# Optimization experiments

Hardware: AMD Instinct MI355X
Metric: run time of the kernel (lower is better)

The kernel has to match this reference:

```python
import jax, jax.numpy as jnp
import numpy as np

H = 12       # heads
D = 768      # hidden size
DH = D // H  # head dim = 64
SCALE = 1.0 / jnp.sqrt(jnp.float32(DH))
LN_EPS = 1e-3  # keras LayerNormalization default epsilon


def setup_inputs() -> dict:
    key = jax.random.key(0)
    ks = jax.random.split(key, 8)
    B, L = 16, 512
    s = 0.02  # truncated-normal-ish init scale
    return {
        "x": jax.random.normal(ks[0], (B, L, D), jnp.float32),
        "mask": jnp.ones((B, L), jnp.int32),
        "Wq": jax.random.normal(ks[1], (D, D), jnp.float32) * s,
        "bq": jnp.zeros((D,), jnp.float32),
        "Wk": jax.random.normal(ks[2], (D, D), jnp.float32) * s,
        "bk": jnp.zeros((D,), jnp.float32),
        "Wv": jax.random.normal(ks[3], (D, D), jnp.float32) * s,
        "bv": jnp.zeros((D,), jnp.float32),
        "Wo": jax.random.normal(ks[4], (D, D), jnp.float32) * s,
        "bo": jnp.zeros((D,), jnp.float32),
        "gamma": jnp.ones((D,), jnp.float32),
        "beta": jnp.zeros((D,), jnp.float32),
    }


def reference(x, mask, Wq, bq, Wk, bk, Wv, bv, Wo, bo, gamma, beta):
    B, L, _ = x.shape
    # QKV projections, split into heads: [B, L, H, DH]
    q = (x @ Wq + bq).reshape(B, L, H, DH)
    k = (x @ Wk + bk).reshape(B, L, H, DH)
    v = (x @ Wv + bv).reshape(B, L, H, DH)
    # scaled dot-product scores: [B, H, Lq, Lk]
    scores = jnp.einsum('bqhd,bkhd->bhqk', q, k) * SCALE
    # key-side padding mask (mask==0 -> -inf)
    neg = jnp.float32(-1e9)
    scores = jnp.where(mask[:, None, None, :] > 0, scores, neg)
    p = jax.nn.softmax(scores, axis=-1)
    # dropout rate fixed to 0.0 -> identity
    ctx = jnp.einsum('bhqk,bkhd->bqhd', p, v).reshape(B, L, D)
    attn_out = ctx @ Wo + bo
    # residual + LayerNorm (keras default eps=1e-3)
    y = x + attn_out
    mu = jnp.mean(y, axis=-1, keepdims=True)
    var = jnp.mean(jnp.square(y - mu), axis=-1, keepdims=True)
    return gamma * (y - mu) * jax.lax.rsqrt(var + LN_EPS) + beta
```

## Files before the change

kernel.cpp:

```cpp
#include <hip/hip_runtime.h>
#include <math.h>

#define NH 12
#define DMODEL 768
#define DHEAD 64
#define BATCH 16
#define SEQ 512
#define NTOK (BATCH*SEQ)
#define ATTN_SCALE 0.125f
#define LN_EPS 1e-3f
#define PADP 72
#define NKT 12

typedef __attribute__((ext_vector_type(8))) short  bf16x8;
typedef __attribute__((ext_vector_type(4))) float  f32x4;

__device__ __forceinline__ unsigned short f2bf(float f) {
    unsigned int u = __float_as_uint(f);
    unsigned int r = (u + 0x7fffu + ((u >> 16) & 1u)) >> 16;
    return (unsigned short)r;
}

__device__ __forceinline__ void async_copy16(const void* g, void* l) {
    __builtin_amdgcn_global_load_lds((const __attribute__((address_space(1))) void*)g,
                                     (__attribute__((address_space(3))) void*)l,
                                     16, 0, 0);
}

#define SBAR() do { \
    __builtin_amdgcn_sched_barrier(0); \
    __builtin_amdgcn_s_barrier(); \
    __builtin_amdgcn_sched_barrier(0); \
} while (0)

#define VMW0() do { \
    __builtin_amdgcn_sched_barrier(0); \
    asm volatile("s_waitcnt vmcnt(0)" ::: "memory"); \
    __builtin_amdgcn_sched_barrier(0); \
} while (0)

__global__ __launch_bounds__(256) void prep_kernel(
    const float* __restrict__ x,
    const float* __restrict__ Wq, const float* __restrict__ Wk,
    const float* __restrict__ Wv, const float* __restrict__ Wo,
    unsigned short* __restrict__ xb,
    unsigned short* __restrict__ tq, unsigned short* __restrict__ tk,
    unsigned short* __restrict__ tv, unsigned short* __restrict__ to_)
{
    __shared__ float tile[32][33];
    const int bid = blockIdx.x;
    const int tid = threadIdx.x;

    if (bid < 6144) {
        int i = (bid * 256 + tid) * 4;
        const float4 v = *(const float4*)(x + i);
        unsigned long long pack =
              (unsigned long long)f2bf(v.x)
            | ((unsigned long long)f2bf(v.y) << 16)
            | ((unsigned long long)f2bf(v.z) << 32)
            | ((unsigned long long)f2bf(v.w) << 48);
        *(unsigned long long*)(xb + i) = pack;
        return;
    }

    const int t   = bid - 6144;
    const int zz  = t / 576;
    const int rem = t % 576;
    const float* W = (zz == 0) ? Wq : (zz == 1) ? Wk : (zz == 2) ? Wv : Wo;
    unsigned short* T = (zz == 0) ? tq : (zz == 1) ? tk : (zz == 2) ? tv : to_;

    const int bx = (rem / 24) * 32;
    const int by = (rem % 24) * 32;
    const int tx = tid & 31, ty = tid >> 5;

    #pragma unroll
    for (int i = 0; i < 32; i += 8)
        tile[ty + i][tx] = W[(size_t)(bx + ty + i) * DMODEL + by + tx];
    __syncthreads();
    #pragma unroll
    for (int i = 0; i < 32; i += 8)
        T[(size_t)(by + ty + i) * DMODEL + bx + tx] = f2bf(tile[tx][ty + i]);
}

#define QSTAGE(kt, sb) do { \
    const int _k0 = (kt) * 64; \
    _Pragma("unroll") \
    for (int _i = 0; _i < 4; ++_i) \
        async_copy16(aSrc + (size_t)_i * (8 * DMODEL) + _k0, &As[sb][(w * 4 + _i) * 512]); \
    _Pragma("unroll") \
    for (int _i = 0; _i < 4; ++_i) \
        async_copy16(bSrc + (size_t)_i * (64 * DMODEL) + _k0, &Bs[sb][(w + 8 * _i) * 512]); \
    if (w < 4) \
        async_copy16(bSrc + (size_t)4 * (64 * DMODEL) + _k0, &Bs[sb][(w + 32) * 512]); \
} while (0)

#define QTILE(t, c, o, hasNext) do { \
    if (hasNext) QSTAGE((t) + 1, o); \
    bf16x8 aF[4][2]; \
    _Pragma("unroll") \
    for (int _m = 0; _m < 4; ++_m) { \
        const int _row = wm * 64 + _m * 16 + l16; \
        aF[_m][0] = *(const bf16x8*)&As[c][_row * 64 + p0]; \
        aF[_m][1] = *(const bf16x8*)&As[c][_row * 64 + (p0 ^ 32)]; \
    } \
    _Pragma("unroll") \
    for (int _nh = 0; _nh < 3; ++_nh) { \
        bf16x8 bF[3][2]; \
        _Pragma("unroll") \
        for (int _n = 0; _n < 3; ++_n) { \
            const int _row = wn * 144 + (_nh * 3 + _n) * 16 + l16; \
            bF[_n][0] = *(const bf16x8*)&Bs[c][_row * 64 + p0]; \
            bF[_n][1] = *(const bf16x8*)&Bs[c][_row * 64 + (p0 ^ 32)]; \
        } \
        __builtin_amdgcn_s_setprio(1); \
        _Pragma("unroll") \
        for (int _k = 0; _k < 2; ++_k) \
          _Pragma("unroll") \
          for (int _m = 0; _m < 4; ++_m) \
            _Pragma("unroll") \
            for (int _n = 0; _n < 3; ++_n) \
              acc[_m][_nh * 3 + _n] = __builtin_amdgcn_mfma_f32_16x16x32_bf16( \
                  aF[_m][_k], bF[_n][_k], acc[_m][_nh * 3 + _n], 0, 0, 0); \
        __builtin_amdgcn_s_setprio(0); \
    } \
    if (hasNext) VMW0(); \
    SBAR(); \
} while (0)

__global__ __launch_bounds__(512, 2) void gemm_db_qkv(
    const unsigned short* __restrict__ xb, const unsigned short* __restrict__ wt,
    const float* __restrict__ bq, const float* __restrict__ bk, const float* __restrict__ bv,
    unsigned short* __restrict__ o0, unsigned short* __restrict__ o1,
    unsigned short* __restrict__ o2)
{
    __shared__ __align__(16) unsigned short As[2][256 * 64];
    __shared__ __align__(16) unsigned short Bs[2][288 * 64];

    const int orig = blockIdx.x;
    const int wg   = (orig & 7) * 32 + (orig >> 3);
    const int m0   = (wg >> 3) * 256;
    const int n0   = (wg & 7) * 288;

    const int tid  = threadIdx.x;
    const int lane = tid & 63;
    const int w    = tid >> 6;
    const int wm   = w >> 1, wn = w & 1;
    const int quad = lane >> 4;
    const int l16  = lane & 15;
    const int rloc = lane >> 3;
    const int csw  = (lane & 7) ^ rloc;
    const int p0   = (quad ^ (l16 & 7)) * 8;

    const unsigned short* aSrc = xb + (size_t)(m0 + w * 32 + rloc) * DMODEL + csw * 8;
    const unsigned short* bSrc = wt + (size_t)(n0 + w * 8  + rloc) * DMODEL + csw * 8;

    f32x4 acc[4][9] = {};

    QSTAGE(0, 0);
    VMW0();
    SBAR();

    #pragma unroll 1
    for (int tt = 0; tt < NKT / 2; ++tt) {
        QTILE(2 * tt,     0, 1, 1);
        QTILE(2 * tt + 1, 1, 0, (tt < NKT / 2 - 1));
    }

    #pragma unroll
    for (int nf = 0; nf < 9; ++nf) {
        const int ncg = n0 + wn * 144 + nf * 16 + l16;
        const int zz  = (ncg >= 1536) ? 2 : (ncg >= 768) ? 1 : 0;
        const int ncl = ncg - zz * 768;
        const int h = ncl >> 6, dh = ncl & 63;
        const float bval = ((zz == 0) ? bq : (zz == 1) ? bk : bv)[ncl];
        if (zz == 2) {
            #pragma unroll
            for (int mi = 0; mi < 4; ++mi) {
                const int mbase = m0 + wm * 64 + mi * 16 + quad * 4;
                const int bi = mbase >> 9, l = mbase & 511;
                unsigned long long pack = 0;
                #pragma unroll
                for (int r = 0; r < 4; ++r)
                    pack |= (unsigned long long)f2bf(acc[mi][nf][r] + bval) << (16 * r);
                *(unsigned long long*)(o2 + ((size_t)((bi * NH + h) * DHEAD + dh)) * SEQ + l) = pack;
            }
        } else {
            const float sc = (zz == 0) ? ATTN_SCALE : 1.0f;
            unsigned short* out = (zz == 0) ? o0 : o1;
            #pragma unroll
            for (int mi = 0; mi < 4; ++mi) {
                const int mbase = m0 + wm * 64 + mi * 16 + quad * 4;
                #pragma unroll
                for (int r = 0; r < 4; ++r) {
                    const int t = mbase + r;
                    const int bi = t >> 9, l = t & 511;
                    out[(size_t)((bi * NH + h) * SEQ + l) * DHEAD + dh] =
                        f2bf((acc[mi][nf][r] + bval) * sc);
                }
            }
        }
    }
}

#define OSTAGE(kt, sb) do { \
    const int _k0 = (kt) * 64; \
    _Pragma("unroll") \
    for (int _i = 0; _i < 2; ++_i) \
        async_copy16(aSrc + (size_t)_i * (8 * DMODEL) + _k0, &Ao[sb][(w * 2 + _i) * 512]); \
    _Pragma("unroll") \
    for (int _i = 0; _i < 3; ++_i) \
        async_copy16(bSrc + (size_t)_i * (8 * DMODEL) + _k0, &Bo[sb][(w * 3 + _i) * 512]); \
} while (0)

#define OTILE(t, c, o, hasNext) do { \
    if (hasNext) OSTAGE((t) + 1, o); \
    bf16x8 aF[4][2], bF[3][2]; \
    _Pragma("unroll") \
    for (int _m = 0; _m < 4; ++_m) { \
        const int _row = wm * 64 + _m * 16 + l16; \
        aF[_m][0] = *(const bf16x8*)&Ao[c][_row * 64 + p0]; \
        aF[_m][1] = *(const bf16x8*)&Ao[c][_row * 64 + (p0 ^ 32)]; \
    } \
    _Pragma("unroll") \
    for (int _n = 0; _n < 3; ++_n) { \
        const int _row = wn * 48 + _n * 16 + l16; \
        bF[_n][0] = *(const bf16x8*)&Bo[c][_row * 64 + p0]; \
        bF[_n][1] = *(const bf16x8*)&Bo[c][_row * 64 + (p0 ^ 32)]; \
    } \
    __builtin_amdgcn_s_setprio(1); \
    _Pragma("unroll") \
    for (int _k = 0; _k < 2; ++_k) \
      _Pragma("unroll") \
      for (int _m = 0; _m < 4; ++_m) \
        _Pragma("unroll") \
        for (int _n = 0; _n < 3; ++_n) \
          acc[_m][_n] = __builtin_amdgcn_mfma_f32_16x16x32_bf16( \
              aF[_m][_k], bF[_n][_k], acc[_m][_n], 0, 0, 0); \
    __builtin_amdgcn_s_setprio(0); \
    if (hasNext) VMW0(); \
    SBAR(); \
} while (0)

__global__ __launch_bounds__(512, 2) void gemm_db_oproj(
    const unsigned short* __restrict__ ctxb, const unsigned short* __restrict__ wto,
    const float* __restrict__ bo, const float* __restrict__ x,
    float* __restrict__ y)
{
    __shared__ __align__(16) unsigned short Ao[2][132 * 64];
    __shared__ __align__(16) unsigned short Bo[2][192 * 64];

    const int orig = blockIdx.x;
    const int wg   = (orig & 7) * 32 + (orig >> 3);
    const int m0   = (wg >> 2) * 128;
    const int n0   = (wg & 3) * 192;

    const int tid  = threadIdx.x;
    const int lane = tid & 63;
    const int w    = tid >> 6;
    const int wm   = w >> 2, wn = w & 3;
    const int quad = lane >> 4;
    const int l16  = lane & 15;
    const int rloc = lane >> 3;
    const int csw  = (lane & 7) ^ rloc;
    const int p0   = (quad ^ (l16 & 7)) * 8;

    const unsigned short* aSrc = ctxb + (size_t)(m0 + w * 16 + rloc) * DMODEL + csw * 8;
    const unsigned short* bSrc = wto  + (size_t)(n0 + w * 24 + rloc) * DMODEL + csw * 8;

    f32x4 acc[4][3] = {};

    OSTAGE(0, 0);
    VMW0();
    SBAR();

    #pragma unroll 1
    for (int tt = 0; tt < NKT / 2; ++tt) {
        OTILE(2 * tt,     0, 1, 1);
        OTILE(2 * tt + 1, 1, 0, (tt < NKT / 2 - 1));
    }

    #pragma unroll
    for (int ni = 0; ni < 3; ++ni) {
        const int ncol = n0 + wn * 48 + ni * 16 + l16;
        const float bv_ = bo[ncol];
        #pragma unroll
        for (int mi = 0; mi < 4; ++mi) {
            const int mbase = m0 + wm * 64 + mi * 16 + quad * 4;
            #pragma unroll
            for (int r = 0; r < 4; ++r) {
                const size_t idx = (size_t)(mbase + r) * DMODEL + ncol;
                y[idx] = acc[mi][ni][r] + bv_ + x[idx];
            }
        }
    }
}

__global__ __launch_bounds__(256, 3) void attn_mfma_kernel(
    const unsigned short* __restrict__ q, const unsigned short* __restrict__ k,
    const unsigned short* __restrict__ vt, const int* __restrict__ mask,
    unsigned short* __restrict__ ctxb)
{
    __shared__ __align__(16) unsigned short Ks[2][64 * 64];
    __shared__ __align__(16) unsigned short Vs[2][64 * 64];
    __shared__ __align__(16) unsigned short Ps[2][64 * PADP];
    __shared__ float maskV[SEQ];

    const int tid  = threadIdx.x;
    const int lane = tid & 63;
    const int w    = tid >> 6;
    const int quad = lane >> 4;
    const int l16  = lane & 15;

    const int id = blockIdx.x;
    const int qt = id / (BATCH * NH);
    const int g  = id % (BATCH * NH);
    const int b  = g / NH, h = g % NH;
    const int q0 = qt * 128;

    const unsigned short* qp  = q  + ((size_t)(b * NH + h) * SEQ + q0) * DHEAD;
    const unsigned short* kp  = k  + (size_t)(b * NH + h) * SEQ * DHEAD;
    const unsigned short* vtp = vt + (size_t)(b * NH + h) * DHEAD * SEQ;

    const int rloc = lane >> 3;
    const int csw  = (lane & 7) ^ rloc;
    const int p0   = (quad ^ (l16 & 7)) * 8;

    #pragma unroll
    for (int ii = 0; ii < 2; ++ii) {
        const int inst = 2 * w + ii;
        async_copy16(kp  + (size_t)(inst * 8 + rloc) * DHEAD + csw * 8, &Ks[0][inst * 512]);
        async_copy16(vtp + (size_t)(inst * 8 + rloc) * SEQ + csw * 8,   &Vs[0][inst * 512]);
    }
    #pragma unroll
    for (int j = 0; j < 2; ++j) {
        const int idx = tid + 256 * j;
        maskV[idx] = (mask[b * SEQ + idx] > 0) ? 0.f : -1e9f;
    }

    bf16x8 aQ[2][2];
    #pragma unroll
    for (int qtl = 0; qtl < 2; ++qtl)
        #pragma unroll
        for (int ks = 0; ks < 2; ++ks)
            aQ[qtl][ks] = *(const bf16x8*)(qp + (size_t)(qtl * 64 + w * 16 + l16) * DHEAD
                                              + ks * 32 + quad * 8);

    bf16x8 ones;
    #pragma unroll
    for (int j = 0; j < 8; ++j) ones[j] = (short)0x3F80;

    f32x4 o[2][4] = {};
    f32x4 lsum[2] = {};
    const f32x4 zf = {0.f, 0.f, 0.f, 0.f};

    __syncthreads();

    #pragma unroll
    for (int it = 0; it < 8; ++it) {
        const int cur = it & 1;
        if (it + 1 < 8) {
            const int kt1 = (it + 1) * 64;
            #pragma unroll
            for (int ii = 0; ii < 2; ++ii) {
                const int inst = 2 * w + ii;
                async_copy16(kp  + (size_t)(kt1 + inst * 8 + rloc) * DHEAD + csw * 8,
                             &Ks[1 - cur][inst * 512]);
                async_copy16(vtp + (size_t)(inst * 8 + rloc) * SEQ + kt1 + csw * 8,
                             &Vs[1 - cur][inst * 512]);
            }
        }
        const int kt = it * 64;

        f32x4 s[2][4];
        #pragma unroll
        for (int ni = 0; ni < 4; ++ni) {
            bf16x8 bK0 = *(const bf16x8*)&Ks[cur][(ni * 16 + l16) * 64 + p0];
            bf16x8 bK1 = *(const bf16x8*)&Ks[cur][(ni * 16 + l16) * 64 + (p0 ^ 32)];
            #pragma unroll
            for (int qtl = 0; qtl < 2; ++qtl) {
                f32x4 t0 = __builtin_amdgcn_mfma_f32_16x16x32_bf16(aQ[qtl][0], bK0, zf, 0, 0, 0);
                s[qtl][ni] = __builtin_amdgcn_mfma_f32_16x16x32_bf16(aQ[qtl][1], bK1, t0, 0, 0, 0);
            }
        }

        #pragma unroll
        for (int ni = 0; ni < 4; ++ni) {
            const float mk = maskV[kt + ni * 16 + l16];
            #pragma unroll
            for (int qtl = 0; qtl < 2; ++qtl)
                #pragma unroll
                for (int r = 0; r < 4; ++r)
                    Ps[qtl][(w * 16 + quad * 4 + r) * PADP + ni * 16 + l16]
                        = (unsigned short)(__float_as_uint(__expf(s[qtl][ni][r] + mk)) >> 16);
        }

        bf16x8 aP[2][2];
        #pragma unroll
        for (int qtl = 0; qtl < 2; ++qtl) {
            #pragma unroll
            for (int ks = 0; ks < 2; ++ks)
                aP[qtl][ks] = *(const bf16x8*)&Ps[qtl][(w * 16 + l16) * PADP + quad * 8 + ks * 32];
            lsum[qtl] = __builtin_amdgcn_mfma_f32_16x16x32_bf16(aP[qtl][0], ones, lsum[qtl], 0, 0, 0);
            lsum[qtl] = __builtin_amdgcn_mfma_f32_16x16x32_bf16(aP[qtl][1], ones, lsum[qtl], 0, 0, 0);
        }

        #pragma unroll
        for (int ni = 0; ni < 4; ++ni) {
            bf16x8 bV0 = *(const bf16x8*)&Vs[cur][(ni * 16 + l16) * 64 + p0];
            bf16x8 bV1 = *(const bf16x8*)&Vs[cur][(ni * 16 + l16) * 64 + (p0 ^ 32)];
            #pragma unroll
            for (int qtl = 0; qtl < 2; ++qtl) {
                o[qtl][ni] = __builtin_amdgcn_mfma_f32_16x16x32_bf16(aP[qtl][0], bV0, o[qtl][ni], 0, 0, 0);
                o[qtl][ni] = __builtin_amdgcn_mfma_f32_16x16x32_bf16(aP[qtl][1], bV1, o[qtl][ni], 0, 0, 0);
            }
        }

        __syncthreads();
    }

    #pragma unroll
    for (int qtl = 0; qtl < 2; ++qtl)
        #pragma unroll
        for (int r = 0; r < 4; ++r) {
            const float inv = 1.f / lsum[qtl][r];
            const int tok = q0 + qtl * 64 + w * 16 + quad * 4 + r;
            #pragma unroll
            for (int ni = 0; ni < 4; ++ni)
                ctxb[(size_t)(b * SEQ + tok) * DMODEL + h * DHEAD + ni * 16 + l16]
                    = f2bf(o[qtl][ni][r] * inv);
        }
}

__global__ __launch_bounds__(256) void ln_kernel(
    const float* __restrict__ y, const float* __restrict__ gamma,
    const float* __restrict__ beta, float* __restrict__ out)
{
    const int t   = blockIdx.x;
    const int tid = threadIdx.x;
    const float* row = y + (size_t)t * DMODEL;

    float vals[3];
    float s = 0.f, s2 = 0.f;
    #pragma unroll
    for (int i = 0; i < 3; ++i) {
        float vv = row[tid + 256 * i];
        vals[i] = vv;
        s  += vv;
        s2 += vv * vv;
    }
    #pragma unroll
    for (int off = 32; off > 0; off >>= 1) {
        s  += __shfl_down(s,  off);
        s2 += __shfl_down(s2, off);
    }
    __shared__ float rbuf[8];
    int w = tid >> 6;
    if ((tid & 63) == 0) { rbuf[w] = s; rbuf[4 + w] = s2; }
    __syncthreads();
    float ts  = rbuf[0] + rbuf[1] + rbuf[2] + rbuf[3];
    float ts2 = rbuf[4] + rbuf[5] + rbuf[6] + rbuf[7];
    float mu  = ts * (1.f / DMODEL);
    float var = ts2 * (1.f / DMODEL) - mu * mu;
    float inv = rsqrtf(var + LN_EPS);
    #pragma unroll
    for (int i = 0; i < 3; ++i) {
        int c = tid + 256 * i;
        out[(size_t)t * DMODEL + c] = gamma[c] * (vals[i] - mu) * inv + beta[c];
    }
}

extern "C" void kernel_launch(void* const* d_in, const int* in_sizes, int n_in,
                              void* d_out, int out_size, void* d_ws, size_t ws_size,
                              hipStream_t stream) {
    const float* x     = (const float*)d_in[0];
    const int*   mask  = (const int*)  d_in[1];
    const float* Wq    = (const float*)d_in[2];
    const float* bq    = (const float*)d_in[3];
    const float* Wk    = (const float*)d_in[4];
    const float* bk    = (const float*)d_in[5];
    const float* Wv    = (const float*)d_in[6];
    const float* bv    = (const float*)d_in[7];
    const float* Wo    = (const float*)d_in[8];
    const float* bo    = (const float*)d_in[9];
    const float* gamma = (const float*)d_in[10];
    const float* beta  = (const float*)d_in[11];
    float* out = (float*)d_out;

    const size_t perTok = (size_t)NTOK * DMODEL;
    const size_t perW   = (size_t)DMODEL * DMODEL;

    unsigned short* xb   = (unsigned short*)d_ws;
    unsigned short* wtq  = xb + perTok;
    unsigned short* wtk  = wtq + perW;
    unsigned short* wtv  = wtk + perW;
    unsigned short* wto  = wtv + perW;
    unsigned short* qb   = wto + perW;
    unsigned short* kb   = qb + perTok;
    unsigned short* vb   = kb + perTok;
    unsigned short* ctxb = vb + perTok;
    float* y = out;

    prep_kernel<<<6144 + 2304, 256, 0, stream>>>(
        x, Wq, Wk, Wv, Wo, xb, wtq, wtk, wtv, wto);

    gemm_db_qkv<<<256, 512, 0, stream>>>(xb, wtq, bq, bk, bv, qb, kb, vb);

    attn_mfma_kernel<<<dim3((SEQ / 128) * BATCH * NH), 256, 0, stream>>>(
        qb, kb, vb, mask, ctxb);

    gemm_db_oproj<<<256, 512, 0, stream>>>(ctxb, wto, bo, x, y);

    ln_kernel<<<NTOK, 256, 0, stream>>>(y, gamma, beta, out);
}
```

Measured before the change: 188.2 us.

## Fuse output projection with residual add and LayerNorm in one kernel

Replaces the separate O-projection GEMM and LayerNorm kernels with one kernel. Each block computes 32 full rows of 768 columns, so the row mean and variance can be reduced in registers and shared memory before the normalized result is written. This removes the round trip of the intermediate y tensor through global memory and one kernel launch. In exchange, every block streams the whole Wo matrix in two 384-column halves, with a smaller A tile per block. The larger shared-memory footprint likely limits occupancy to one block per CU.

```diff
diff --git a/kernel.cpp b/kernel.cpp
--- a/kernel.cpp
+++ b/kernel.cpp
@@ -202,97 +202,157 @@
     }
 }
 
-#define OSTAGE(kt, sb) do { \
-    const int _k0 = (kt) * 64; \
-    _Pragma("unroll") \
-    for (int _i = 0; _i < 2; ++_i) \
-        async_copy16(aSrc + (size_t)_i * (8 * DMODEL) + _k0, &Ao[sb][(w * 2 + _i) * 512]); \
-    _Pragma("unroll") \
-    for (int _i = 0; _i < 3; ++_i) \
-        async_copy16(bSrc + (size_t)_i * (8 * DMODEL) + _k0, &Bo[sb][(w * 3 + _i) * 512]); \
-} while (0)
-
-#define OTILE(t, c, o, hasNext) do { \
-    if (hasNext) OSTAGE((t) + 1, o); \
-    bf16x8 aF[4][2], bF[3][2]; \
-    _Pragma("unroll") \
-    for (int _m = 0; _m < 4; ++_m) { \
-        const int _row = wm * 64 + _m * 16 + l16; \
-        aF[_m][0] = *(const bf16x8*)&Ao[c][_row * 64 + p0]; \
-        aF[_m][1] = *(const bf16x8*)&Ao[c][_row * 64 + (p0 ^ 32)]; \
+#define FSTAGE_B(kb, h, pb) do { \
+    _Pragma("unroll") \
+    for (int _i = 0; _i < 6; ++_i) \
+        async_copy16(wto + (size_t)((h) * 384 + _i * 64 + w * 8 + rloc) * DMODEL + (kb) * 64 + csw * 8, \
+                     &Bb[pb][(_i * 64 + w * 8) * 64]); \
+} while (0)
+
+#define FSTAGE_A(kb, ab) do { \
+    if (w < 4) \
+        async_copy16(ctxb + (size_t)(m0 + w * 8 + rloc) * DMODEL + (kb) * 64 + csw * 8, \
+                     &Ab[ab][(w * 8) * 64]); \
+} while (0)
+
+#define FPHASE(h, pb, ab) do { \
+    bf16x8 aF[2][2], bF[3][2]; \
+    _Pragma("unroll") \
+    for (int _m = 0; _m < 2; ++_m) { \
+        const int _row = _m * 16 + l16; \
+        aF[_m][0] = *(const bf16x8*)&Ab[ab][_row * 64 + p0]; \
+        aF[_m][1] = *(const bf16x8*)&Ab[ab][_row * 64 + (p0 ^ 32)]; \
     } \
     _Pragma("unroll") \
     for (int _n = 0; _n < 3; ++_n) { \
-        const int _row = wn * 48 + _n * 16 + l16; \
-        bF[_n][0] = *(const bf16x8*)&Bo[c][_row * 64 + p0]; \
-        bF[_n][1] = *(const bf16x8*)&Bo[c][_row * 64 + (p0 ^ 32)]; \
+        const int _row = w * 48 + _n * 16 + l16; \
+        bF[_n][0] = *(const bf16x8*)&Bb[pb][_row * 64 + p0]; \
+        bF[_n][1] = *(const bf16x8*)&Bb[pb][_row * 64 + (p0 ^ 32)]; \
     } \
     __builtin_amdgcn_s_setprio(1); \
     _Pragma("unroll") \
     for (int _k = 0; _k < 2; ++_k) \
       _Pragma("unroll") \
-      for (int _m = 0; _m < 4; ++_m) \
+      for (int _m = 0; _m < 2; ++_m) \
         _Pragma("unroll") \
         for (int _n = 0; _n < 3; ++_n) \
-          acc[_m][_n] = __builtin_amdgcn_mfma_f32_16x16x32_bf16( \
-              aF[_m][_k], bF[_n][_k], acc[_m][_n], 0, 0, 0); \
+          acc[_m][(h) * 3 + _n] = __builtin_amdgcn_mfma_f32_16x16x32_bf16( \
+              aF[_m][_k], bF[_n][_k], acc[_m][(h) * 3 + _n], 0, 0, 0); \
     __builtin_amdgcn_s_setprio(0); \
-    if (hasNext) VMW0(); \
-    SBAR(); \
-} while (0)
-
-__global__ __launch_bounds__(512, 2) void gemm_db_oproj(
+} while (0)
+
+__global__ __launch_bounds__(512, 2) void oproj_ln_fused(
     const unsigned short* __restrict__ ctxb, const unsigned short* __restrict__ wto,
     const float* __restrict__ bo, const float* __restrict__ x,
-    float* __restrict__ y)
+    const float* __restrict__ gamma, const float* __restrict__ beta,
+    float* __restrict__ out)
 {
-    __shared__ __align__(16) unsigned short Ao[2][132 * 64];
-    __shared__ __align__(16) unsigned short Bo[2][192 * 64];
-
-    const int orig = blockIdx.x;
-    const int wg   = (orig & 7) * 32 + (orig >> 3);
-    const int m0   = (wg >> 2) * 128;
-    const int n0   = (wg & 3) * 192;
-
+    __shared__ __align__(16) unsigned short Bb[2][384 * 64];
+    __shared__ __align__(16) unsigned short Ab[2][32 * 64];
+    __shared__ float rs[32][8], rs2[32][8];
+
+    const int m0   = blockIdx.x * 32;
     const int tid  = threadIdx.x;
     const int lane = tid & 63;
     const int w    = tid >> 6;
-    const int wm   = w >> 2, wn = w & 3;
     const int quad = lane >> 4;
     const int l16  = lane & 15;
     const int rloc = lane >> 3;
     const int csw  = (lane & 7) ^ rloc;
     const int p0   = (quad ^ (l16 & 7)) * 8;
 
-    const unsigned short* aSrc = ctxb + (size_t)(m0 + w * 16 + rloc) * DMODEL + csw * 8;
-    const unsigned short* bSrc = wto  + (size_t)(n0 + w * 24 + rloc) * DMODEL + csw * 8;
-
-    f32x4 acc[4][3] = {};
-
-    OSTAGE(0, 0);
+    f32x4 acc[2][6] = {};
+
+    FSTAGE_B(0, 0, 0);
+    FSTAGE_A(0, 0);
     VMW0();
     SBAR();
 
     #pragma unroll 1
-    for (int tt = 0; tt < NKT / 2; ++tt) {
-        OTILE(2 * tt,     0, 1, 1);
-        OTILE(2 * tt + 1, 1, 0, (tt < NKT / 2 - 1));
-    }
-
-    #pragma unroll
-    for (int ni = 0; ni < 3; ++ni) {
-        const int ncol = n0 + wn * 48 + ni * 16 + l16;
-        const float bv_ = bo[ncol];
-        #pragma unroll
-        for (int mi = 0; mi < 4; ++mi) {
-            const int mbase = m0 + wm * 64 + mi * 16 + quad * 4;
-            #pragma unroll
-            for (int r = 0; r < 4; ++r) {
-                const size_t idx = (size_t)(mbase + r) * DMODEL + ncol;
-                y[idx] = acc[mi][ni][r] + bv_ + x[idx];
-            }
-        }
-    }
+    for (int kb = 0; kb < NKT; ++kb) {
+        FSTAGE_B(kb, 1, 1);
+        if (kb + 1 < NKT) FSTAGE_A(kb + 1, (kb + 1) & 1);
+        FPHASE(0, 0, kb & 1);
+        VMW0();
+        SBAR();
+        if (kb + 1 < NKT) {
+            FSTAGE_B(kb + 1, 0, 0);
+            FPHASE(1, 1, kb & 1);
+            VMW0();
+            SBAR();
+        } else {
+            FPHASE(1, 1, kb & 1);
+        }
+    }
+
+    float yv[2][6][4];
+    float sp[2][4] = {}, sp2[2][4] = {};
+    #pragma unroll
+    for (int mi = 0; mi < 2; ++mi)
+        #pragma unroll
+        for (int j = 0; j < 6; ++j) {
+            const int col = (j >= 3 ? 384 : 0) + w * 48 + (j % 3) * 16 + l16;
+            const float bv_ = bo[col];
+            #pragma unroll
+            for (int rr = 0; rr < 4; ++rr) {
+                const int row = mi * 16 + quad * 4 + rr;
+                const float v = acc[mi][j][rr] + bv_
+                              + x[(size_t)(m0 + row) * DMODEL + col];
+                yv[mi][j][rr] = v;
+                sp[mi][rr]  += v;
+                sp2[mi][rr] += v * v;
+            }
+        }
+
+    #pragma unroll
+    for (int off = 1; off < 16; off <<= 1)
+        #pragma unroll
+        for (int mi = 0; mi < 2; ++mi)
+            #pragma unroll
+            for (int rr = 0; rr < 4; ++rr) {
+                sp[mi][rr]  += __shfl_xor(sp[mi][rr],  off);
+                sp2[mi][rr] += __shfl_xor(sp2[mi][rr], off);
+            }
+
+    if (l16 == 0)
+        #pragma unroll
+        for (int mi = 0; mi < 2; ++mi)
+            #pragma unroll
+            for (int rr = 0; rr < 4; ++rr) {
+                const int row = mi * 16 + quad * 4 + rr;
+                rs[row][w]  = sp[mi][rr];
+                rs2[row][w] = sp2[mi][rr];
+            }
+    __syncthreads();
+
+    float mu_[2][4], inv_[2][4];
+    #pragma unroll
+    for (int mi = 0; mi < 2; ++mi)
+        #pragma unroll
+        for (int rr = 0; rr < 4; ++rr) {
+            const int row = mi * 16 + quad * 4 + rr;
+            float ts = 0.f, ts2 = 0.f;
+            #pragma unroll
+            for (int ww = 0; ww < 8; ++ww) { ts += rs[row][ww]; ts2 += rs2[row][ww]; }
+            const float mu  = ts * (1.f / DMODEL);
+            const float var = ts2 * (1.f / DMODEL) - mu * mu;
+            mu_[mi][rr]  = mu;
+            inv_[mi][rr] = rsqrtf(var + LN_EPS);
+        }
+
+    #pragma unroll
+    for (int mi = 0; mi < 2; ++mi)
+        #pragma unroll
+        for (int j = 0; j < 6; ++j) {
+            const int col = (j >= 3 ? 384 : 0) + w * 48 + (j % 3) * 16 + l16;
+            const float gm = gamma[col], bt = beta[col];
+            #pragma unroll
+            for (int rr = 0; rr < 4; ++rr) {
+                const int row = mi * 16 + quad * 4 + rr;
+                out[(size_t)(m0 + row) * DMODEL + col] =
+                    gm * (yv[mi][j][rr] - mu_[mi][rr]) * inv_[mi][rr] + bt;
+            }
+        }
 }
 
 __global__ __launch_bounds__(256, 3) void attn_mfma_kernel(
@@ -429,44 +489,6 @@
                 ctxb[(size_t)(b * SEQ + tok) * DMODEL + h * DHEAD + ni * 16 + l16]
                     = f2bf(o[qtl][ni][r] * inv);
         }
-}
-
-__global__ __launch_bounds__(256) void ln_kernel(
-    const float* __restrict__ y, const float* __restrict__ gamma,
-    const float* __restrict__ beta, float* __restrict__ out)
-{
-    const int t   = blockIdx.x;
-    const int tid = threadIdx.x;
-    const float* row = y + (size_t)t * DMODEL;
-
-    float vals[3];
-    float s = 0.f, s2 = 0.f;
-    #pragma unroll
-    for (int i = 0; i < 3; ++i) {
-        float vv = row[tid + 256 * i];
-        vals[i] = vv;
-        s  += vv;
-        s2 += vv * vv;
-    }
-    #pragma unroll
-    for (int off = 32; off > 0; off >>= 1) {
-        s  += __shfl_down(s,  off);
-        s2 += __shfl_down(s2, off);
-    }
-    __shared__ float rbuf[8];
-    int w = tid >> 6;
-    if ((tid & 63) == 0) { rbuf[w] = s; rbuf[4 + w] = s2; }
-    __syncthreads();
-    float ts  = rbuf[0] + rbuf[1] + rbuf[2] + rbuf[3];
-    float ts2 = rbuf[4] + rbuf[5] + rbuf[6] + rbuf[7];
-    float mu  = ts * (1.f / DMODEL);
-    float var = ts2 * (1.f / DMODEL) - mu * mu;
-    float inv = rsqrtf(var + LN_EPS);
-    #pragma unroll
-    for (int i = 0; i < 3; ++i) {
-        int c = tid + 256 * i;
-        out[(size_t)t * DMODEL + c] = gamma[c] * (vals[i] - mu) * inv + beta[c];
-    }
 }
 
 extern "C" void kernel_launch(void* const* d_in, const int* in_sizes, int n_in,
@@ -498,7 +520,6 @@
     unsigned short* kb   = qb + perTok;
     unsigned short* vb   = kb + perTok;
     unsigned short* ctxb = vb + perTok;
-    float* y = out;
 
     prep_kernel<<<6144 + 2304, 256, 0, stream>>>(
         x, Wq, Wk, Wv, Wo, xb, wtq, wtk, wtv, wto);
@@ -508,7 +529,6 @@
     attn_mfma_kernel<<<dim3((SEQ / 128) * BATCH * NH), 256, 0, stream>>>(
         qb, kb, vb, mask, ctxb);
 
-    gemm_db_oproj<<<256, 512, 0, stream>>>(ctxb, wto, bo, x, y);
-
-    ln_kernel<<<NTOK, 256, 0, stream>>>(y, gamma, beta, out);
-}
+    oproj_ln_fused<<<256, 512, 0, stream>>>(
+        ctxb, wto, bo, x, gamma, beta, out);
+}
```

New measurement: 191.8 us. No clear change (+1.9%).

## Replace double-buffered QKV GEMM with single-buffered smaller-M tile for occupancy

Applied to the files above, without the earlier changes.

The QKV projection GEMM drops its double-buffered 256x288 tile for a single-buffered 128x288 tile and launches 512 workgroups instead of 256. Launch bounds go from 2 to 4 waves-per-EU and LDS per block falls from about 139KB to about 53KB, so more blocks can share a CU and the wider grid fills more CUs. In exchange the kernel loses the overlap of global-to-LDS loads with MFMA work and adds a second barrier per k-step, relying on other resident blocks to hide latency. Each block also reloads the 288-row weight tile for half as many rows, doubling B-operand traffic.

```diff
diff --git a/kernel.cpp b/kernel.cpp
--- a/kernel.cpp
+++ b/kernel.cpp
@@ -82,63 +82,29 @@
         T[(size_t)(by + ty + i) * DMODEL + bx + tx] = f2bf(tile[tx][ty + i]);
 }
 
-#define QSTAGE(kt, sb) do { \
+#define QSTAGE(kt) do { \
     const int _k0 = (kt) * 64; \
+    async_copy16(aSrc + _k0,              &As[(2 * w)     * 512]); \
+    async_copy16(aSrc + 8 * DMODEL + _k0, &As[(2 * w + 1) * 512]); \
     _Pragma("unroll") \
     for (int _i = 0; _i < 4; ++_i) \
-        async_copy16(aSrc + (size_t)_i * (8 * DMODEL) + _k0, &As[sb][(w * 4 + _i) * 512]); \
-    _Pragma("unroll") \
-    for (int _i = 0; _i < 4; ++_i) \
-        async_copy16(bSrc + (size_t)_i * (64 * DMODEL) + _k0, &Bs[sb][(w + 8 * _i) * 512]); \
+        async_copy16(bSrc + (size_t)_i * (64 * DMODEL) + _k0, &Bs[(w + 8 * _i) * 512]); \
     if (w < 4) \
-        async_copy16(bSrc + (size_t)4 * (64 * DMODEL) + _k0, &Bs[sb][(w + 32) * 512]); \
+        async_copy16(bSrc2 + _k0, &Bs[(w + 32) * 512]); \
 } while (0)
 
-#define QTILE(t, c, o, hasNext) do { \
-    if (hasNext) QSTAGE((t) + 1, o); \
-    bf16x8 aF[4][2]; \
-    _Pragma("unroll") \
-    for (int _m = 0; _m < 4; ++_m) { \
-        const int _row = wm * 64 + _m * 16 + l16; \
-        aF[_m][0] = *(const bf16x8*)&As[c][_row * 64 + p0]; \
-        aF[_m][1] = *(const bf16x8*)&As[c][_row * 64 + (p0 ^ 32)]; \
-    } \
-    _Pragma("unroll") \
-    for (int _nh = 0; _nh < 3; ++_nh) { \
-        bf16x8 bF[3][2]; \
-        _Pragma("unroll") \
-        for (int _n = 0; _n < 3; ++_n) { \
-            const int _row = wn * 144 + (_nh * 3 + _n) * 16 + l16; \
-            bF[_n][0] = *(const bf16x8*)&Bs[c][_row * 64 + p0]; \
-            bF[_n][1] = *(const bf16x8*)&Bs[c][_row * 64 + (p0 ^ 32)]; \
-        } \
-        __builtin_amdgcn_s_setprio(1); \
-        _Pragma("unroll") \
-        for (int _k = 0; _k < 2; ++_k) \
-          _Pragma("unroll") \
-          for (int _m = 0; _m < 4; ++_m) \
-            _Pragma("unroll") \
-            for (int _n = 0; _n < 3; ++_n) \
-              acc[_m][_nh * 3 + _n] = __builtin_amdgcn_mfma_f32_16x16x32_bf16( \
-                  aF[_m][_k], bF[_n][_k], acc[_m][_nh * 3 + _n], 0, 0, 0); \
-        __builtin_amdgcn_s_setprio(0); \
-    } \
-    if (hasNext) VMW0(); \
-    SBAR(); \
-} while (0)
-
-__global__ __launch_bounds__(512, 2) void gemm_db_qkv(
+__global__ __launch_bounds__(512, 4) void gemm_sb_qkv(
     const unsigned short* __restrict__ xb, const unsigned short* __restrict__ wt,
     const float* __restrict__ bq, const float* __restrict__ bk, const float* __restrict__ bv,
     unsigned short* __restrict__ o0, unsigned short* __restrict__ o1,
     unsigned short* __restrict__ o2)
 {
-    __shared__ __align__(16) unsigned short As[2][256 * 64];
-    __shared__ __align__(16) unsigned short Bs[2][288 * 64];
+    __shared__ __align__(16) unsigned short As[128 * 64];
+    __shared__ __align__(16) unsigned short Bs[288 * 64];
 
     const int orig = blockIdx.x;
-    const int wg   = (orig & 7) * 32 + (orig >> 3);
-    const int m0   = (wg >> 3) * 256;
+    const int wg   = (orig & 7) * 64 + (orig >> 3);
+    const int m0   = (wg >> 3) * 128;
     const int n0   = (wg & 7) * 288;
 
     const int tid  = threadIdx.x;
@@ -151,19 +117,47 @@
     const int csw  = (lane & 7) ^ rloc;
     const int p0   = (quad ^ (l16 & 7)) * 8;
 
-    const unsigned short* aSrc = xb + (size_t)(m0 + w * 32 + rloc) * DMODEL + csw * 8;
-    const unsigned short* bSrc = wt + (size_t)(n0 + w * 8  + rloc) * DMODEL + csw * 8;
-
-    f32x4 acc[4][9] = {};
-
-    QSTAGE(0, 0);
-    VMW0();
-    SBAR();
+    const unsigned short* aSrc  = xb + (size_t)(m0 + 16 * w + rloc) * DMODEL + csw * 8;
+    const unsigned short* bSrc  = wt + (size_t)(n0 + 8 * w + rloc) * DMODEL + csw * 8;
+    const unsigned short* bSrc2 = wt + (size_t)(n0 + 256 + 8 * w + rloc) * DMODEL + csw * 8;
+
+    f32x4 acc[2][9] = {};
 
     #pragma unroll 1
-    for (int tt = 0; tt < NKT / 2; ++tt) {
-        QTILE(2 * tt,     0, 1, 1);
-        QTILE(2 * tt + 1, 1, 0, (tt < NKT / 2 - 1));
+    for (int kb = 0; kb < NKT; ++kb) {
+        QSTAGE(kb);
+        VMW0();
+        SBAR();
+
+        bf16x8 aF[2][2];
+        #pragma unroll
+        for (int mi = 0; mi < 2; ++mi) {
+            const int row = wm * 32 + mi * 16 + l16;
+            aF[mi][0] = *(const bf16x8*)&As[row * 64 + p0];
+            aF[mi][1] = *(const bf16x8*)&As[row * 64 + (p0 ^ 32)];
+        }
+        #pragma unroll
+        for (int nh = 0; nh < 3; ++nh) {
+            bf16x8 bF[3][2];
+            #pragma unroll
+            for (int n = 0; n < 3; ++n) {
+                const int row = wn * 144 + (nh * 3 + n) * 16 + l16;
+                bF[n][0] = *(const bf16x8*)&Bs[row * 64 + p0];
+                bF[n][1] = *(const bf16x8*)&Bs[row * 64 + (p0 ^ 32)];
+            }
+            __builtin_amdgcn_s_setprio(1);
+            #pragma unroll
+            for (int k = 0; k < 2; ++k)
+                #pragma unroll
+                for (int mi = 0; mi < 2; ++mi)
+                    #pragma unroll
+                    for (int n = 0; n < 3; ++n)
+                        acc[mi][nh * 3 + n] = __builtin_amdgcn_mfma_f32_16x16x32_bf16(
+                            aF[mi][k], bF[n][k], acc[mi][nh * 3 + n], 0, 0, 0);
+            __builtin_amdgcn_s_setprio(0);
+        }
+
+        if (kb < NKT - 1) SBAR();
     }
 
     #pragma unroll
@@ -175,8 +169,8 @@
         const float bval = ((zz == 0) ? bq : (zz == 1) ? bk : bv)[ncl];
         if (zz == 2) {
             #pragma unroll
-            for (int mi = 0; mi < 4; ++mi) {
-                const int mbase = m0 + wm * 64 + mi * 16 + quad * 4;
+            for (int mi = 0; mi < 2; ++mi) {
+                const int mbase = m0 + wm * 32 + mi * 16 + quad * 4;
                 const int bi = mbase >> 9, l = mbase & 511;
                 unsigned long long pack = 0;
                 #pragma unroll
@@ -188,8 +182,8 @@
             const float sc = (zz == 0) ? ATTN_SCALE : 1.0f;
             unsigned short* out = (zz == 0) ? o0 : o1;
             #pragma unroll
-            for (int mi = 0; mi < 4; ++mi) {
-                const int mbase = m0 + wm * 64 + mi * 16 + quad * 4;
+            for (int mi = 0; mi < 2; ++mi) {
+                const int mbase = m0 + wm * 32 + mi * 16 + quad * 4;
                 #pragma unroll
                 for (int r = 0; r < 4; ++r) {
                     const int t = mbase + r;
@@ -206,10 +200,10 @@
     const int _k0 = (kt) * 64; \
     _Pragma("unroll") \
     for (int _i = 0; _i < 2; ++_i) \
-        async_copy16(aSrc + (size_t)_i * (8 * DMODEL) + _k0, &Ao[sb][(w * 2 + _i) * 512]); \
+        async_copy16(aSrcO + (size_t)_i * (8 * DMODEL) + _k0, &Ao[sb][(w * 2 + _i) * 512]); \
     _Pragma("unroll") \
     for (int _i = 0; _i < 3; ++_i) \
-        async_copy16(bSrc + (size_t)_i * (8 * DMODEL) + _k0, &Bo[sb][(w * 3 + _i) * 512]); \
+        async_copy16(bSrcO + (size_t)_i * (8 * DMODEL) + _k0, &Bo[sb][(w * 3 + _i) * 512]); \
 } while (0)
 
 #define OTILE(t, c, o, hasNext) do { \
@@ -264,8 +258,8 @@
     const int csw  = (lane & 7) ^ rloc;
     const int p0   = (quad ^ (l16 & 7)) * 8;
 
-    const unsigned short* aSrc = ctxb + (size_t)(m0 + w * 16 + rloc) * DMODEL + csw * 8;
-    const unsigned short* bSrc = wto  + (size_t)(n0 + w * 24 + rloc) * DMODEL + csw * 8;
+    const unsigned short* aSrcO = ctxb + (size_t)(m0 + w * 16 + rloc) * DMODEL + csw * 8;
+    const unsigned short* bSrcO = wto  + (size_t)(n0 + w * 24 + rloc) * DMODEL + csw * 8;
 
     f32x4 acc[4][3] = {};
 
@@ -503,12 +497,12 @@
     prep_kernel<<<6144 + 2304, 256, 0, stream>>>(
         x, Wq, Wk, Wv, Wo, xb, wtq, wtk, wtv, wto);
 
-    gemm_db_qkv<<<256, 512, 0, stream>>>(xb, wtq, bq, bk, bv, qb, kb, vb);
+    gemm_sb_qkv<<<512, 512, 0, stream>>>(xb, wtq, bq, bk, bv, qb, kb, vb);
 
     attn_mfma_kernel<<<dim3((SEQ / 128) * BATCH * NH), 256, 0, stream>>>(
         qb, kb, vb, mask, ctxb);
 
-    gemm_db_oproj<<<256, 512, 0, stream>>>(ctxb, wto, bo, x, y);
+    gemm_db_oproj<<<dim3(256), 512, 0, stream>>>(ctxb, wto, bo, x, y);
 
     ln_kernel<<<NTOK, 256, 0, stream>>>(y, gamma, beta, out);
 }
```

Result: slower. 197.2 us (+4.8%).
